# Kernel optimization log

Hardware: AMD Instinct MI355X
Metric: run time of the kernel (lower is better)

Reference implementation:

```python
import jax, jax.numpy as jnp
import numpy as np

NUM_FRAMES = 257  # init_kwargs num_frames
K = 5             # number of keyframes


def setup_inputs() -> dict:
    key = jax.random.key(0)
    k1, k2, k3 = jax.random.split(key, 3)
    latents = jax.random.normal(k1, (K, 1, 128, 32, 32), dtype=jnp.float32)
    strengths = jax.random.uniform(k2, (K,), dtype=jnp.float32)
    # unique sorted frame indices in [0, NUM_FRAMES) (original skips duplicate segments)
    frame_indices = jnp.sort(
        jax.random.choice(k3, NUM_FRAMES, (K,), replace=False)
    ).astype(jnp.int32)
    return {"latents": latents, "strengths": strengths, "frame_indices": frame_indices}


def reference(latents, strengths, frame_indices):
    """Vectorized equivalent of MultiKeyframeProcessor.process_keyframes
    (interpolation_mode='linear').

    latents:       [K, B, C, H, W] sorted by frame_indices
    strengths:     [K]
    frame_indices: [K] int, sorted, unique, all < NUM_FRAMES
    Returns (conditioning_latents [B,C,T,H,W], conditioning_masks [B,T]).
    """
    T = NUM_FRAMES
    fi = frame_indices
    Kk = fi.shape[0]
    t = jnp.arange(T, dtype=jnp.int32)
    # index of last keyframe with frame_index <= t (-1 means before first keyframe)
    j = jnp.searchsorted(fi, t, side="right") - 1
    j0 = jnp.clip(j, 0, Kk - 1)
    j1 = jnp.clip(j + 1, 0, Kk - 1)

    fif = fi.astype(jnp.float32)
    tf = t.astype(jnp.float32)

    before = t < fi[0]
    after = t > fi[-1]
    at_kf = fi[j0] == t  # frame coincides with a keyframe (false when before)
    interior = ~(before | after | at_kf)

    denom = jnp.maximum(fif[j1] - fif[j0], 1.0)
    alpha = (tf - fif[j0]) / denom  # linear interpolation weight
    w1 = jnp.where(interior, alpha, 0.0)   # weight for next keyframe
    w0 = 1.0 - w1                          # weight for previous keyframe

    # --- conditioning masks (per-frame strength) ---
    m_mid = w0 * strengths[j0] + w1 * strengths[j1]  # covers interior and at_kf
    decay_before = jnp.maximum(1.0 - (fif[0] - tf) / jnp.maximum(fif[0], 1.0), 0.0)
    decay_after = jnp.maximum(1.0 - (tf - fif[-1]) / (T - fif[-1]), 0.0)
    mask_t = jnp.where(before, strengths[0] * decay_before,
             jnp.where(after, strengths[-1] * decay_after, m_mid))  # [T]

    # --- conditioning latents ---
    # before: j0==0, w1==0 -> first latent; after: j0==j1==K-1, w1==0 -> last latent
    lat0 = latents[j0]  # [T, B, C, H, W]
    lat1 = latents[j1]  # [T, B, C, H, W]
    out = w0[:, None, None, None, None] * lat0 + w1[:, None, None, None, None] * lat1
    conditioning_latents = jnp.moveaxis(out, 0, 2)  # [B, C, T, H, W]

    B = latents.shape[1]
    conditioning_masks = jnp.broadcast_to(mask_t[None, :], (B, T))
    return conditioning_latents, conditioning_masks
```

## Files before the change

kernel.cpp:

```cpp
#include <hip/hip_runtime.h>


#define T_FRAMES 257
#define KK 5
#define PER_KEY 131072
#define HW 1024
#define LAT_OUT 33685504
#define TGROUPS 16
#define TLEN 17

typedef float f32x4 __attribute__((ext_vector_type(4)));

__global__ __launch_bounds__(256) void mkp_kernel(
    const float* __restrict__ lat,
    const float* __restrict__ str,
    const int* __restrict__ fi,
    float* __restrict__ out)
{
    const int b   = blockIdx.x;
    const int tid = threadIdx.x;
    const int g   = b >> 7;
    const int c   = b & 127;

    int   fiv[KK];
    float sv[KK];
#pragma unroll
    for (int k = 0; k < KK; ++k) { fiv[k] = fi[k]; sv[k] = str[k]; }

    f32x4 kf[KK];
#pragma unroll
    for (int k = 0; k < KK; ++k)
        kf[k] = *((const f32x4*)(lat + k * PER_KEY + c * HW) + tid);

    const int t0 = g * TLEN;
    const int t1 = (t0 + TLEN < T_FRAMES) ? t0 + TLEN : T_FRAMES;

    float* po = out + c * (T_FRAMES * HW);

    for (int t = t0; t < t1; ++t) {
        int j = -1;
#pragma unroll
        for (int k = 0; k < KK; ++k) j += (fiv[k] <= t) ? 1 : 0;
        const int j0 = (j < 0) ? 0 : j;
        const int j1 = (j + 1 > KK - 1) ? KK - 1 : j + 1;

        const bool before   = t < fiv[0];
        const bool after    = t > fiv[KK - 1];
        const bool at_kf    = (fiv[j0] == t);
        const bool interior = !(before || after || at_kf);

        const float tf    = (float)t;
        const float fj0   = (float)fiv[j0];
        const float fj1   = (float)fiv[j1];
        const float denom = fmaxf(fj1 - fj0, 1.0f);
        const float alpha = (tf - fj0) / denom;
        const float w1    = interior ? alpha : 0.0f;
        const float w0    = 1.0f - w1;

        float wk[KK];
#pragma unroll
        for (int k = 0; k < KK; ++k)
            wk[k] = ((k == j0) ? w0 : 0.0f) + ((k == j1) ? w1 : 0.0f);

        f32x4 r = kf[0] * wk[0];
#pragma unroll
        for (int k = 1; k < KK; ++k) {
            r.x = fmaf(kf[k].x, wk[k], r.x);
            r.y = fmaf(kf[k].y, wk[k], r.y);
            r.z = fmaf(kf[k].z, wk[k], r.z);
            r.w = fmaf(kf[k].w, wk[k], r.w);
        }

        *((f32x4*)(po + t * HW) + tid) = r;
    }

    if (c == 0 && tid < (t1 - t0)) {
        const int t = t0 + tid;
        int j = -1;
#pragma unroll
        for (int k = 0; k < KK; ++k) j += (fiv[k] <= t) ? 1 : 0;
        const int j0 = (j < 0) ? 0 : j;
        const int j1 = (j + 1 > KK - 1) ? KK - 1 : j + 1;

        const bool before   = t < fiv[0];
        const bool after    = t > fiv[KK - 1];
        const bool at_kf    = (fiv[j0] == t);
        const bool interior = !(before || after || at_kf);

        const float tf    = (float)t;
        const float fj0   = (float)fiv[j0];
        const float fj1   = (float)fiv[j1];
        const float denom = fmaxf(fj1 - fj0, 1.0f);
        const float alpha = (tf - fj0) / denom;
        const float w1    = interior ? alpha : 0.0f;
        const float w0    = 1.0f - w1;

        float m;
        if (before) {
            const float f0f = (float)fiv[0];
            m = sv[0] * fmaxf(1.0f - (f0f - tf) / fmaxf(f0f, 1.0f), 0.0f);
        } else if (after) {
            const float fLf = (float)fiv[KK - 1];
            m = sv[KK - 1] * fmaxf(1.0f - (tf - fLf) / ((float)T_FRAMES - fLf), 0.0f);
        } else {
            m = w0 * sv[j0] + w1 * sv[j1];
        }
        out[LAT_OUT + t] = m;
    }
}

extern "C" void kernel_launch(void* const* d_in, const int* in_sizes, int n_in,
                              void* d_out, int out_size, void* d_ws, size_t ws_size,
                              hipStream_t stream)
{
    const float* lat = (const float*)d_in[0];
    const float* str = (const float*)d_in[1];
    const int*   fi  = (const int*)d_in[2];
    float* out = (float*)d_out;

    const int grid = TGROUPS * 128;
    mkp_kernel<<<grid, 256, 0, stream>>>(lat, str, fi, out);
}
```

Before: 144.8 us.

## Assign each wave a full channel plane across 32 frames, shrinking grid to 256 blocks

```diff
diff --git a/kernel.cpp b/kernel.cpp
--- a/kernel.cpp
+++ b/kernel.cpp
@@ -6,8 +6,6 @@
 #define PER_KEY 131072
 #define HW 1024
 #define LAT_OUT 33685504
-#define TGROUPS 16
-#define TLEN 17
 
 typedef float f32x4 __attribute__((ext_vector_type(4)));
 
@@ -17,24 +15,31 @@
     const int* __restrict__ fi,
     float* __restrict__ out)
 {
-    const int b   = blockIdx.x;
-    const int tid = threadIdx.x;
-    const int g   = b >> 7;
-    const int c   = b & 127;
+    const int b    = blockIdx.x;
+    const int tid  = threadIdx.x;
+    const int c    = b & 127;
+    const int h    = b >> 7;
+    const int w    = tid >> 6;
+    const int lane = tid & 63;
 
     int   fiv[KK];
     float sv[KK];
 #pragma unroll
     for (int k = 0; k < KK; ++k) { fiv[k] = fi[k]; sv[k] = str[k]; }
 
-    f32x4 kf[KK];
+    f32x4 kf[KK][4];
 #pragma unroll
-    for (int k = 0; k < KK; ++k)
-        kf[k] = *((const f32x4*)(lat + k * PER_KEY + c * HW) + tid);
+    for (int k = 0; k < KK; ++k) {
+        const f32x4* src = (const f32x4*)(lat + k * PER_KEY + c * HW);
+#pragma unroll
+        for (int q = 0; q < 4; ++q)
+            kf[k][q] = src[q * 64 + lane];
+    }
 
-    const int t0 = g * TLEN;
-    const int t1 = (t0 + TLEN < T_FRAMES) ? t0 + TLEN : T_FRAMES;
+    const int t0 = h * 128 + w * 32;
+    const int t1 = (h == 1 && w == 3) ? 257 : t0 + 32;
 
+    const float* dummy; (void)dummy;
     float* po = out + c * (T_FRAMES * HW);
 
     for (int t = t0; t < t1; ++t) {
@@ -62,20 +67,24 @@
         for (int k = 0; k < KK; ++k)
             wk[k] = ((k == j0) ? w0 : 0.0f) + ((k == j1) ? w1 : 0.0f);
 
-        f32x4 r = kf[0] * wk[0];
+        f32x4* plane4 = (f32x4*)(po + t * HW);
 #pragma unroll
-        for (int k = 1; k < KK; ++k) {
-            r.x = fmaf(kf[k].x, wk[k], r.x);
-            r.y = fmaf(kf[k].y, wk[k], r.y);
-            r.z = fmaf(kf[k].z, wk[k], r.z);
-            r.w = fmaf(kf[k].w, wk[k], r.w);
+        for (int q = 0; q < 4; ++q) {
+            f32x4 r = kf[0][q] * wk[0];
+#pragma unroll
+            for (int k = 1; k < KK; ++k) {
+                r.x = fmaf(kf[k][q].x, wk[k], r.x);
+                r.y = fmaf(kf[k][q].y, wk[k], r.y);
+                r.z = fmaf(kf[k][q].z, wk[k], r.z);
+                r.w = fmaf(kf[k][q].w, wk[k], r.w);
+            }
+            plane4[q * 64 + lane] = r;
         }
-
-        *((f32x4*)(po + t * HW) + tid) = r;
     }
 
-    if (c == 0 && tid < (t1 - t0)) {
-        const int t = t0 + tid;
+    const int nmask = (h == 0) ? 128 : 129;
+    if (c == 0 && tid < nmask) {
+        const int t = h * 128 + tid;
         int j = -1;
 #pragma unroll
         for (int k = 0; k < KK; ++k) j += (fiv[k] <= t) ? 1 : 0;
@@ -118,6 +127,6 @@
     const int*   fi  = (const int*)d_in[2];
     float* out = (float*)d_out;
 
-    const int grid = TGROUPS * 128;
+    const int grid = 256;
     mkp_kernel<<<grid, 256, 0, stream>>>(lat, str, fi, out);
 }
```

After: 140.7 us. -2.8%, faster.
